# Performance work log

Measured on AMD Instinct MI355X. Metric: run time of the kernel, lower is better.

Reference implementation:

```python
import math
import jax, jax.numpy as jnp
import numpy as np

D_MODEL = 1024
D_CTX = 1024
NUM_HEADS = 16
ATTN_DIM = 1024
HEAD_DIM = ATTN_DIM // NUM_HEADS  # 64
ROPE_GAMMA = 10.0
ROTARY_BASE = 10000.0
ATTN_SCALE = math.sqrt(ATTN_DIM)  # note: module scales by sqrt(attn_dim), not sqrt(head_dim)


def _apply_rope(x, cos, sin):
    # x: [H,B,T,D]; cos/sin: [1,B,T,D//2]
    half = x.shape[-1] // 2
    x1, x2 = x[..., :half], x[..., half:]
    return jnp.concatenate([x1 * cos - x2 * sin, x1 * sin + x2 * cos], axis=-1)


def setup_inputs() -> dict:
    key = jax.random.key(0)
    ks = jax.random.split(key, 12)
    B, T, L = 4, 1024, 1024
    x = jax.random.normal(ks[0], (B, D_MODEL, T), jnp.float32)
    context = jax.random.normal(ks[1], (B, L, D_CTX), jnp.float32)
    # prefix (padding) masks with per-example valid lengths, as in real padded batches
    lens_q = jnp.array([1024, 896, 768, 640])
    lens_k = jnp.array([1024, 960, 832, 704])
    x_mask = (jnp.arange(T)[None, :] < lens_q[:, None]).astype(jnp.int32)[:, None, :]  # [B,1,T]
    context_mask = (jnp.arange(L)[None, :] < lens_k[:, None]).astype(jnp.int32)[:, None, :]  # [B,1,L]
    s = 0.02
    Wq = jax.random.normal(ks[2], (D_MODEL, ATTN_DIM), jnp.float32) * s
    bq = jax.random.normal(ks[3], (ATTN_DIM,), jnp.float32) * s
    Wk = jax.random.normal(ks[4], (D_CTX, ATTN_DIM), jnp.float32) * s
    bk = jax.random.normal(ks[5], (ATTN_DIM,), jnp.float32) * s
    Wv = jax.random.normal(ks[6], (D_CTX, ATTN_DIM), jnp.float32) * s
    bv = jax.random.normal(ks[7], (ATTN_DIM,), jnp.float32) * s
    Wo = jax.random.normal(ks[8], (ATTN_DIM, D_MODEL), jnp.float32) * s
    bo = jax.random.normal(ks[9], (D_MODEL,), jnp.float32) * s
    return {"x": x, "context": context, "x_mask": x_mask, "context_mask": context_mask,
            "Wq": Wq, "bq": bq, "Wk": Wk, "bk": bk, "Wv": Wv, "bv": bv, "Wo": Wo, "bo": bo}


def reference(x, context, x_mask, context_mask, Wq, bq, Wk, bk, Wv, bv, Wo, bo):
    B, _, T = x.shape
    L = context.shape[1]
    H, D = NUM_HEADS, HEAD_DIM
    xm = x_mask.astype(jnp.float32)          # [B,1,T]
    cmf = context_mask.astype(jnp.float32)   # [B,1,L]

    q = jnp.swapaxes(x, 1, 2) @ Wq + bq      # [B,T,attn_dim]
    k = context @ Wk + bk                    # [B,L,attn_dim]
    v = context @ Wv + bv                    # [B,L,attn_dim]

    q = q.reshape(B, T, H, D).transpose(2, 0, 1, 3)  # [H,B,T,D]
    k = k.reshape(B, L, H, D).transpose(2, 0, 1, 3)  # [H,B,L,D]
    v = v.reshape(B, L, H, D).transpose(2, 0, 1, 3)  # [H,B,L,D]

    # length-normalized RoPE (LARoPE)
    len_q = xm.sum(axis=(-2, -1)).reshape(-1, 1, 1)   # [B,1,1]
    len_k = cmf.sum(axis=(-2, -1)).reshape(-1, 1, 1)  # [B,1,1]
    pos_q = jnp.arange(T, dtype=jnp.float32).reshape(1, -1, 1)
    pos_k = jnp.arange(L, dtype=jnp.float32).reshape(1, -1, 1)
    inv_freq = 1.0 / (ROTARY_BASE ** (jnp.arange(0, D, 2, dtype=jnp.float32) / D))
    theta = (inv_freq * ROPE_GAMMA).reshape(1, 1, -1)  # [1,1,D//2]
    freqs_q = (pos_q / len_q) * theta  # [B,T,D//2]
    freqs_k = (pos_k / len_k) * theta  # [B,L,D//2]
    q = _apply_rope(q, jnp.cos(freqs_q)[None], jnp.sin(freqs_q)[None])
    k = _apply_rope(k, jnp.cos(freqs_k)[None], jnp.sin(freqs_k)[None])

    logits = jnp.einsum('hbtd,hbld->hbtl', q, k) / ATTN_SCALE  # [H,B,T,L]
    key_pad = (context_mask == 0)[None]  # [1,B,1,L]
    logits = jnp.where(key_pad, -jnp.inf, logits)
    attn = jax.nn.softmax(logits, axis=-1)
    query_pad = (x_mask == 0).transpose(1, 0, 2)[..., None]  # [1,B,T,1]
    attn = jnp.where(query_pad, 0.0, attn)

    out = jnp.einsum('hbtl,hbld->hbtd', attn, v)          # [H,B,T,D]
    out = out.transpose(1, 2, 0, 3).reshape(B, T, ATTN_DIM)
    out = out @ Wo + bo                                   # [B,T,d_model]
    out = out * jnp.swapaxes(xm, 1, 2)                    # [B,T,1] broadcast
    return jnp.swapaxes(out, 1, 2)                        # [B,d_model,T]
```

## Files before the change

### kernel.cpp

```cpp
#include <hip/hip_runtime.h>
#include <hip/hip_bf16.h>

typedef __attribute__((ext_vector_type(8))) short s8v;
typedef __attribute__((ext_vector_type(4))) float f4v;
typedef __attribute__((ext_vector_type(4))) unsigned short u4v;
typedef __attribute__((ext_vector_type(2))) unsigned int u2v;

#define NH 16

__device__ __forceinline__ unsigned short f2bf(float f) {
  union { float f; unsigned int u; } v; v.f = f;
  unsigned int r = (v.u + 0x7fffu + ((v.u >> 16) & 1u)) >> 16;
  return (unsigned short)r;
}
__device__ __forceinline__ void gll16(const void* g, void* l) {
  __builtin_amdgcn_global_load_lds((const __attribute__((address_space(1))) void*)g,
                                   (__attribute__((address_space(3))) void*)l, 16, 0, 0);
}
__device__ __forceinline__ unsigned int cvtpk(float lo, float hi) {
  unsigned int r;
  asm volatile("v_cvt_pk_bf16_f32 %0, %1, %2" : "=v"(r) : "v"(lo), "v"(hi));
  return r;
}

__global__ __launch_bounds__(256) void prep_kernel(
    const float* __restrict__ x, const float* __restrict__ ctx,
    const float* __restrict__ Wq, const float* __restrict__ Wk,
    const float* __restrict__ Wv, const float* __restrict__ Wo,
    const int* __restrict__ xm, const int* __restrict__ cm,
    unsigned short* __restrict__ xT, unsigned short* __restrict__ ctxb,
    unsigned short* __restrict__ WqT, unsigned short* __restrict__ WkT,
    unsigned short* __restrict__ WvT, unsigned short* __restrict__ WoT,
    float* __restrict__ lens, float2* __restrict__ rope) {
  const int z = blockIdx.z;
  const int tid = threadIdx.x;
  if (z == 12) {
    if (blockIdx.x | blockIdx.y) return;
    const int w = tid >> 6, lane = tid & 63;
    const int g = w * 2 + (lane >> 5);
    const int l32 = lane & 31;
    const int* m = (g < 4) ? (xm + g * 1024) : (cm + (g - 4) * 1024);
    int s = 0;
    for (int i = l32; i < 1024; i += 32) s += m[i];
    for (int o = 16; o; o >>= 1) s += __shfl_xor(s, o);
    if (l32 == 0) lens[g] = (float)s;
    return;
  }
  if (z == 13) {
    const int idx = blockIdx.y * 32 + blockIdx.x;
    if (idx >= 256) return;
    const int which = idx >> 7;
    const int b = (idx >> 5) & 3;
    const int t0 = (idx & 31) * 32;
    const int* m = (which ? cm : xm) + b * 1024;
    const int lane = tid & 63;
    int s = 0;
    for (int i = lane; i < 1024; i += 64) s += m[i];
    for (int o = 32; o; o >>= 1) s += __shfl_xor(s, o);
    const float len = (float)s;
    const int j = tid & 31;
    const float theta = 10.0f * __expf((float)j * -0.28782313662425572f);
    float2* rt = rope + ((size_t)(which * 4 + b) << 15);
    for (int it = 0; it < 4; ++it) {
      const int t = t0 + (tid >> 5) + it * 8;
      const float fr = (float)t / len * theta;
      float sn, cs;
      __sincosf(fr, &sn, &cs);
      rt[t * 32 + j] = make_float2(cs, sn);
    }
    return;
  }
  if (z >= 8) {
    const float* in = ctx + ((size_t)(z - 8) << 20);
    unsigned short* out = ctxb + ((size_t)(z - 8) << 20);
    const int i = (blockIdx.y * 32 + blockIdx.x) * 1024 + tid * 4;
    const f4v v = *(const f4v*)&in[i];
    u4v o;
#pragma unroll
    for (int j = 0; j < 4; ++j) o[j] = f2bf(v[j]);
    *(u4v*)&out[i] = o;
    return;
  }
  __shared__ unsigned short tile[32][33];
  const float* in;
  unsigned short* out;
  if (z < 4)      { in = x + ((size_t)z << 20); out = xT + ((size_t)z << 20); }
  else if (z == 4){ in = Wq; out = WqT; }
  else if (z == 5){ in = Wk; out = WkT; }
  else if (z == 6){ in = Wv; out = WvT; }
  else            { in = Wo; out = WoT; }
  const int r0 = blockIdx.y * 32, c0 = blockIdx.x * 32;
  const int tx = tid & 31, ty = tid >> 5;
  for (int i = ty; i < 32; i += 8) tile[i][tx] = f2bf(in[(size_t)(r0 + i) * 1024 + c0 + tx]);
  __syncthreads();
  for (int i = ty; i < 32; i += 8) out[(size_t)(c0 + i) * 1024 + r0 + tx] = tile[tx][i];
}

__global__ __launch_bounds__(256) void gemm_qkv_kernel(
    const unsigned short* __restrict__ xT, const unsigned short* __restrict__ ctxb,
    const unsigned short* __restrict__ WqT, const unsigned short* __restrict__ WkT,
    const unsigned short* __restrict__ WvT,
    const float* __restrict__ bq, const float* __restrict__ bk, const float* __restrict__ bv,
    unsigned short* __restrict__ Qb, unsigned short* __restrict__ Kb,
    unsigned short* __restrict__ Vtb, const float2* __restrict__ rope) {
  __shared__ __attribute__((aligned(16))) unsigned short As[8192];
  __shared__ __attribute__((aligned(16))) unsigned short Bs[8192];
  const int id = blockIdx.x + (blockIdx.y << 3) + (blockIdx.z << 8);
  const int rest = id >> 3;
  const int my = (id & 7) + ((rest & 3) << 3);
  const int nx = (rest >> 2) & 7;
  const int mode = rest >> 5;
  const unsigned short* A  = (mode == 0) ? xT : ctxb;
  const unsigned short* Bt = (mode == 0) ? WqT : (mode == 1) ? WkT : WvT;
  const float* bias        = (mode == 0) ? bq : (mode == 1) ? bk : bv;
  const int tid = threadIdx.x;
  const int lane = tid & 63, w = tid >> 6;
  const int lq = lane & 15, lg = lane >> 4;
  const int m0 = my * 128, n0 = nx * 128;
  const int wm = (w & 1) * 64, wn = (w >> 1) * 64;
  const int cswz = (lq & 7) << 3;
  f4v acc[4][4] = {};

  for (int kt = 0; kt < 16; ++kt) {
    const int k0 = kt * 64;
#pragma unroll
    for (int i = 0; i < 4; ++i) {
      const int ci = i * 256 + tid;
      const int row = ci >> 3;
      const int col = ((ci & 7) * 8) ^ ((row & 7) << 3);
      gll16(&A[(size_t)(m0 + row) * 1024 + k0 + col], &As[ci * 8]);
      gll16(&Bt[(size_t)(n0 + row) * 1024 + k0 + col], &Bs[ci * 8]);
    }
    __syncthreads();
#pragma unroll
    for (int kc = 0; kc < 2; ++kc) {
      s8v af[4], bfr[4];
#pragma unroll
      for (int i = 0; i < 4; ++i)
        af[i] = *(const s8v*)&As[(wm + i * 16 + lq) * 64 + ((kc * 32 + lg * 8) ^ cswz)];
#pragma unroll
      for (int i = 0; i < 4; ++i)
        bfr[i] = *(const s8v*)&Bs[(wn + i * 16 + lq) * 64 + ((kc * 32 + lg * 8) ^ cswz)];
#pragma unroll
      for (int mi = 0; mi < 4; ++mi)
#pragma unroll
        for (int ni = 0; ni < 4; ++ni)
          acc[mi][ni] = __builtin_amdgcn_mfma_f32_16x16x32_bf16(af[mi], bfr[ni], acc[mi][ni], 0, 0, 0);
    }
    __syncthreads();
  }

  float bv4[4];
#pragma unroll
  for (int ni = 0; ni < 4; ++ni) bv4[ni] = bias[n0 + wn + ni * 16 + lq];
  const int b = m0 >> 10;

  if (mode <= 1) {
    unsigned short* O = mode ? Kb : Qb;
    const float2* rt = rope + ((size_t)(mode * 4 + b) << 15);
    const int h = (n0 + wn) >> 6;
#pragma unroll
    for (int mi = 0; mi < 4; ++mi) {
#pragma unroll
      for (int rr = 0; rr < 4; ++rr) {
        const int m = m0 + wm + mi * 16 + lg * 4 + rr;
        const int t = m & 1023;
#pragma unroll
        for (int ni = 0; ni < 2; ++ni) {
          const int jj = ni * 16 + lq;
          const float2 cs2 = rt[t * 32 + jj];
          const float x1 = acc[mi][ni][rr] + bv4[ni];
          const float x2 = acc[mi][ni + 2][rr] + bv4[ni + 2];
          unsigned short* bp = &O[((size_t)((b * NH + h) * 1024 + t)) * 64 + jj];
          bp[0] = f2bf(x1 * cs2.x - x2 * cs2.y);
          bp[32] = f2bf(x1 * cs2.y + x2 * cs2.x);
        }
      }
    }
  } else {
#pragma unroll
    for (int mi = 0; mi < 4; ++mi) {
      const int mbase = m0 + wm + mi * 16 + lg * 4;
      const int l0 = mbase & 1023;
#pragma unroll
      for (int ni = 0; ni < 4; ++ni) {
        const int n = n0 + wn + ni * 16 + lq;
        const int hh = n >> 6, d = n & 63;
        u4v pk;
#pragma unroll
        for (int rr = 0; rr < 4; ++rr) pk[rr] = f2bf(acc[mi][ni][rr] + bv4[ni]);
        *(u4v*)&Vtb[((size_t)((b * NH + hh) * 64 + d)) * 1024 + l0] = pk;
      }
    }
  }
}

__global__ __launch_bounds__(256) void gemm_o_kernel(
    const unsigned short* __restrict__ A, const unsigned short* __restrict__ Bt,
    const float* __restrict__ bias, float* __restrict__ Cout,
    const int* __restrict__ xmask) {
  __shared__ __attribute__((aligned(16))) unsigned short As[8192];
  __shared__ __attribute__((aligned(16))) unsigned short Bs[8192];
  const int id = blockIdx.x + (blockIdx.y << 3);
  const int rest = id >> 3;
  const int my = (id & 7) + ((rest & 3) << 3);
  const int nx = rest >> 2;
  const int tid = threadIdx.x;
  const int lane = tid & 63, w = tid >> 6;
  const int lq = lane & 15, lg = lane >> 4;
  const int m0 = my * 128, n0 = nx * 128;
  const int wm = (w & 1) * 64, wn = (w >> 1) * 64;
  const int cswz = (lq & 7) << 3;
  f4v acc[4][4] = {};

  for (int kt = 0; kt < 16; ++kt) {
    const int k0 = kt * 64;
#pragma unroll
    for (int i = 0; i < 4; ++i) {
      const int ci = i * 256 + tid;
      const int row = ci >> 3;
      const int col = ((ci & 7) * 8) ^ ((row & 7) << 3);
      gll16(&A[(size_t)(m0 + row) * 1024 + k0 + col], &As[ci * 8]);
      gll16(&Bt[(size_t)(n0 + row) * 1024 + k0 + col], &Bs[ci * 8]);
    }
    __syncthreads();
#pragma unroll
    for (int kc = 0; kc < 2; ++kc) {
      s8v af[4], bfr[4];
#pragma unroll
      for (int i = 0; i < 4; ++i)
        af[i] = *(const s8v*)&As[(wm + i * 16 + lq) * 64 + ((kc * 32 + lg * 8) ^ cswz)];
#pragma unroll
      for (int i = 0; i < 4; ++i)
        bfr[i] = *(const s8v*)&Bs[(wn + i * 16 + lq) * 64 + ((kc * 32 + lg * 8) ^ cswz)];
#pragma unroll
      for (int mi = 0; mi < 4; ++mi)
#pragma unroll
        for (int ni = 0; ni < 4; ++ni)
          acc[mi][ni] = __builtin_amdgcn_mfma_f32_16x16x32_bf16(af[mi], bfr[ni], acc[mi][ni], 0, 0, 0);
    }
    __syncthreads();
  }

  float bv4[4];
#pragma unroll
  for (int ni = 0; ni < 4; ++ni) bv4[ni] = bias[n0 + wn + ni * 16 + lq];
  const int b = m0 >> 10;
#pragma unroll
  for (int mi = 0; mi < 4; ++mi) {
    const int mbase = m0 + wm + mi * 16 + lg * 4;
    const int t0 = mbase & 1023;
#pragma unroll
    for (int ni = 0; ni < 4; ++ni) {
      const int n = n0 + wn + ni * 16 + lq;
      f4v pk;
#pragma unroll
      for (int rr = 0; rr < 4; ++rr) {
        float v = acc[mi][ni][rr] + bv4[ni];
        v *= (float)xmask[b * 1024 + t0 + rr];
        pk[rr] = v;
      }
      *(f4v*)&Cout[(size_t)b * 1024 * 1024 + (size_t)n * 1024 + t0] = pk;
    }
  }
}

__global__ __launch_bounds__(512) void attn_kernel(
    const unsigned short* __restrict__ Q, const unsigned short* __restrict__ K,
    const unsigned short* __restrict__ Vt, const float* __restrict__ lens,
    unsigned short* __restrict__ Aout) {
  __shared__ __attribute__((aligned(16))) unsigned short Ks[2][4096];
  __shared__ __attribute__((aligned(16))) unsigned short Vs[2][4096];
  __shared__ __attribute__((aligned(16))) unsigned short Plds[8][16][72];
  const int tid = threadIdx.x;
  const int lane = tid & 63, w = tid >> 6;
  const int lq = lane & 15, lg = lane >> 4;
  const int id = blockIdx.x + (blockIdx.y << 3);
  const int bh = (id & 7) + (((id >> 3) & 7) << 3);
  const int qblk = id >> 6;
  const int b = bh >> 4, h = bh & 15;
  const int lenq = (int)lens[b];
  if (qblk * 128 >= lenq) return;
  const int lenk = (int)lens[4 + b];
  const int nkt = (lenk + 63) >> 6;
  const int qrow = qblk * 128 + w * 16;
  const unsigned short* Qp = Q + ((size_t)bh * 1024 + qrow) * 64;
  const unsigned short* Kp = K + (size_t)bh * 65536;
  const unsigned short* Vp = Vt + (size_t)bh * 65536;
  const s8v qf0 = *(const s8v*)&Qp[lq * 64 + lg * 8];
  const s8v qf1 = *(const s8v*)&Qp[lq * 64 + 32 + lg * 8];
  const int r0 = tid >> 3;
  const int c0x = ((tid & 7) * 8) ^ ((r0 & 7) << 3);
  const int cswz = (lq & 7) << 3;

  gll16(&Kp[(size_t)r0 * 64 + c0x], &Ks[0][tid * 8]);
  gll16(&Vp[(size_t)r0 * 1024 + c0x], &Vs[0][tid * 8]);
  __syncthreads();

  const float SC2 = 0.0450842200277f;
  float m_run = -1e30f, s_run = 0.0f;
  f4v ot[4] = {};
  for (int kt = 0; kt < nkt; ++kt) {
    const int p = kt & 1;
    if (kt + 1 < nkt) {
      const int kn = (kt + 1) * 64;
      gll16(&Kp[(size_t)(kn + r0) * 64 + c0x], &Ks[p ^ 1][tid * 8]);
      gll16(&Vp[(size_t)r0 * 1024 + kn + c0x], &Vs[p ^ 1][tid * 8]);
    }
    const int k0 = kt * 64;
    const bool full = (k0 + 64 <= lenk);
    float pvv[16];
    float tmax = -1e30f;
    __builtin_amdgcn_s_setprio(1);
#pragma unroll
    for (int kk = 0; kk < 4; ++kk) {
      const int krow = kk * 16 + lq;
      const s8v a0 = *(const s8v*)&Ks[p][krow * 64 + ((lg * 8) ^ cswz)];
      const s8v a1 = *(const s8v*)&Ks[p][krow * 64 + ((32 + lg * 8) ^ cswz)];
      f4v s = {};
      s = __builtin_amdgcn_mfma_f32_16x16x32_bf16(a0, qf0, s, 0, 0, 0);
      s = __builtin_amdgcn_mfma_f32_16x16x32_bf16(a1, qf1, s, 0, 0, 0);
#pragma unroll
      for (int rr = 0; rr < 4; ++rr) {
        float v = s[rr] * SC2;
        if (!full) {
          const int key = k0 + kk * 16 + lg * 4 + rr;
          if (key >= lenk) v = -1e30f;
        }
        pvv[kk * 4 + rr] = v;
        tmax = fmaxf(tmax, v);
      }
    }
    __builtin_amdgcn_s_setprio(0);
    tmax = fmaxf(tmax, __shfl_xor(tmax, 16));
    tmax = fmaxf(tmax, __shfl_xor(tmax, 32));
    if (__any(tmax > m_run + 8.0f)) {
      const float m_new = fmaxf(m_run, tmax);
      const float alpha = exp2f(m_run - m_new);
#pragma unroll
      for (int d = 0; d < 4; ++d)
#pragma unroll
        for (int j = 0; j < 4; ++j) ot[d][j] *= alpha;
      s_run *= alpha;
      m_run = m_new;
    }
    float psum = 0.0f;
#pragma unroll
    for (int kk = 0; kk < 4; ++kk) {
      const float e0 = exp2f(pvv[kk * 4 + 0] - m_run);
      const float e1 = exp2f(pvv[kk * 4 + 1] - m_run);
      const float e2 = exp2f(pvv[kk * 4 + 2] - m_run);
      const float e3 = exp2f(pvv[kk * 4 + 3] - m_run);
      psum += (e0 + e1) + (e2 + e3);
      u2v pw;
      pw[0] = cvtpk(e0, e1);
      pw[1] = cvtpk(e2, e3);
      *(u2v*)&Plds[w][lq][kk * 16 + lg * 4] = pw;
    }
    psum += __shfl_xor(psum, 16);
    psum += __shfl_xor(psum, 32);
    s_run += psum;
    const s8v pb0 = *(const s8v*)&Plds[w][lq][lg * 8];
    const s8v pb1 = *(const s8v*)&Plds[w][lq][32 + lg * 8];
    __builtin_amdgcn_s_setprio(1);
#pragma unroll
    for (int d = 0; d < 4; ++d) {
      const int vrow = d * 16 + lq;
      const s8v av0 = *(const s8v*)&Vs[p][vrow * 64 + ((lg * 8) ^ cswz)];
      const s8v av1 = *(const s8v*)&Vs[p][vrow * 64 + ((32 + lg * 8) ^ cswz)];
      ot[d] = __builtin_amdgcn_mfma_f32_16x16x32_bf16(av0, pb0, ot[d], 0, 0, 0);
      ot[d] = __builtin_amdgcn_mfma_f32_16x16x32_bf16(av1, pb1, ot[d], 0, 0, 0);
    }
    __builtin_amdgcn_s_setprio(0);
    if (kt + 1 < nkt) __syncthreads();
  }
  const float inv = 1.0f / s_run;
  const int t = qrow + lq;
  unsigned short* op = Aout + ((size_t)(b * 1024 + t)) * 1024 + h * 64;
#pragma unroll
  for (int d = 0; d < 4; ++d) {
    u4v oo;
#pragma unroll
    for (int rr = 0; rr < 4; ++rr) oo[rr] = f2bf(ot[d][rr] * inv);
    *(u4v*)&op[d * 16 + lg * 4] = oo;
  }
}

extern "C" void kernel_launch(void* const* d_in, const int* in_sizes, int n_in,
                              void* d_out, int out_size, void* d_ws, size_t ws_size,
                              hipStream_t stream) {
  const float* x   = (const float*)d_in[0];
  const float* ctx = (const float*)d_in[1];
  const int* xm = (const int*)d_in[2];
  const int* cm = (const int*)d_in[3];
  const float* Wq = (const float*)d_in[4];
  const float* bq = (const float*)d_in[5];
  const float* Wk = (const float*)d_in[6];
  const float* bk = (const float*)d_in[7];
  const float* Wv = (const float*)d_in[8];
  const float* bv = (const float*)d_in[9];
  const float* Wo = (const float*)d_in[10];
  const float* bo = (const float*)d_in[11];

  char* ws = (char*)d_ws;
  const size_t MB = 1024 * 1024;
  unsigned short* xT   = (unsigned short*)(ws);
  unsigned short* AOb  = (unsigned short*)(ws);
  unsigned short* ctxb = (unsigned short*)(ws + 8 * MB);
  unsigned short* WqT  = (unsigned short*)(ws + 16 * MB);
  unsigned short* WkT  = (unsigned short*)(ws + 18 * MB);
  unsigned short* WvT  = (unsigned short*)(ws + 20 * MB);
  unsigned short* WoT  = (unsigned short*)(ws + 22 * MB);
  unsigned short* Qb   = (unsigned short*)(ws + 24 * MB);
  unsigned short* Kb   = (unsigned short*)(ws + 32 * MB);
  unsigned short* Vtb  = (unsigned short*)(ws + 40 * MB);
  float* lens          = (float*)(ws + 48 * MB);
  float2* rope         = (float2*)(ws + 49 * MB);

  prep_kernel<<<dim3(32, 32, 14), 256, 0, stream>>>(x, ctx, Wq, Wk, Wv, Wo, xm, cm,
                                                    xT, ctxb, WqT, WkT, WvT, WoT, lens, rope);
  gemm_qkv_kernel<<<dim3(8, 32, 3), 256, 0, stream>>>(xT, ctxb, WqT, WkT, WvT,
                                                      bq, bk, bv, Qb, Kb, Vtb, rope);
  attn_kernel<<<dim3(8, 64), 512, 0, stream>>>(Qb, Kb, Vtb, lens, AOb);
  gemm_o_kernel<<<dim3(8, 32), 256, 0, stream>>>(AOb, WoT, bo, (float*)d_out, xm);
}
```

Before: 123.9 us.

## Double-buffer LDS tiles in QKV and output projection GEMMs

Both projection GEMM kernels now use two LDS buffers. The next K-tile's global-to-LDS loads are issued before the MFMA work on the current tile, so load latency can overlap with compute and one barrier per iteration is removed. LDS use per block doubles to 64KB, which may lower occupancy. Correctness relies on the remaining end-of-loop barrier and on the compiler waiting for the async loads before that barrier.

```diff
diff --git a/kernel.cpp b/kernel.cpp
--- a/kernel.cpp
+++ b/kernel.cpp
@@ -103,8 +103,8 @@
     const float* __restrict__ bq, const float* __restrict__ bk, const float* __restrict__ bv,
     unsigned short* __restrict__ Qb, unsigned short* __restrict__ Kb,
     unsigned short* __restrict__ Vtb, const float2* __restrict__ rope) {
-  __shared__ __attribute__((aligned(16))) unsigned short As[8192];
-  __shared__ __attribute__((aligned(16))) unsigned short Bs[8192];
+  __shared__ __attribute__((aligned(16))) unsigned short As[2][8192];
+  __shared__ __attribute__((aligned(16))) unsigned short Bs[2][8192];
   const int id = blockIdx.x + (blockIdx.y << 3) + (blockIdx.z << 8);
   const int rest = id >> 3;
   const int my = (id & 7) + ((rest & 3) << 3);
@@ -119,28 +119,38 @@
   const int m0 = my * 128, n0 = nx * 128;
   const int wm = (w & 1) * 64, wn = (w >> 1) * 64;
   const int cswz = (lq & 7) << 3;
+  const int srow = tid >> 3;
+  const int scol = ((tid & 7) * 8) ^ ((srow & 7) << 3);
+  const unsigned short* Ap = A + (size_t)(m0 + srow) * 1024 + scol;
+  const unsigned short* Bp = Bt + (size_t)(n0 + srow) * 1024 + scol;
   f4v acc[4][4] = {};
 
+#pragma unroll
+  for (int i = 0; i < 4; ++i) {
+    gll16(Ap + i * 32 * 1024, &As[0][(i * 256 + tid) * 8]);
+    gll16(Bp + i * 32 * 1024, &Bs[0][(i * 256 + tid) * 8]);
+  }
+  __syncthreads();
+
   for (int kt = 0; kt < 16; ++kt) {
-    const int k0 = kt * 64;
-#pragma unroll
-    for (int i = 0; i < 4; ++i) {
-      const int ci = i * 256 + tid;
-      const int row = ci >> 3;
-      const int col = ((ci & 7) * 8) ^ ((row & 7) << 3);
-      gll16(&A[(size_t)(m0 + row) * 1024 + k0 + col], &As[ci * 8]);
-      gll16(&Bt[(size_t)(n0 + row) * 1024 + k0 + col], &Bs[ci * 8]);
-    }
-    __syncthreads();
+    const int cur = kt & 1;
+    if (kt + 1 < 16) {
+      const int kn = (kt + 1) * 64;
+#pragma unroll
+      for (int i = 0; i < 4; ++i) {
+        gll16(Ap + i * 32 * 1024 + kn, &As[cur ^ 1][(i * 256 + tid) * 8]);
+        gll16(Bp + i * 32 * 1024 + kn, &Bs[cur ^ 1][(i * 256 + tid) * 8]);
+      }
+    }
 #pragma unroll
     for (int kc = 0; kc < 2; ++kc) {
       s8v af[4], bfr[4];
 #pragma unroll
       for (int i = 0; i < 4; ++i)
-        af[i] = *(const s8v*)&As[(wm + i * 16 + lq) * 64 + ((kc * 32 + lg * 8) ^ cswz)];
+        af[i] = *(const s8v*)&As[cur][(wm + i * 16 + lq) * 64 + ((kc * 32 + lg * 8) ^ cswz)];
 #pragma unroll
       for (int i = 0; i < 4; ++i)
-        bfr[i] = *(const s8v*)&Bs[(wn + i * 16 + lq) * 64 + ((kc * 32 + lg * 8) ^ cswz)];
+        bfr[i] = *(const s8v*)&Bs[cur][(wn + i * 16 + lq) * 64 + ((kc * 32 + lg * 8) ^ cswz)];
 #pragma unroll
       for (int mi = 0; mi < 4; ++mi)
 #pragma unroll
@@ -199,8 +209,8 @@
     const unsigned short* __restrict__ A, const unsigned short* __restrict__ Bt,
     const float* __restrict__ bias, float* __restrict__ Cout,
     const int* __restrict__ xmask) {
-  __shared__ __attribute__((aligned(16))) unsigned short As[8192];
-  __shared__ __attribute__((aligned(16))) unsigned short Bs[8192];
+  __shared__ __attribute__((aligned(16))) unsigned short As[2][8192];
+  __shared__ __attribute__((aligned(16))) unsigned short Bs[2][8192];
   const int id = blockIdx.x + (blockIdx.y << 3);
   const int rest = id >> 3;
   const int my = (id & 7) + ((rest & 3) << 3);
@@ -211,28 +221,38 @@
   const int m0 = my * 128, n0 = nx * 128;
   const int wm = (w & 1) * 64, wn = (w >> 1) * 64;
   const int cswz = (lq & 7) << 3;
+  const int srow = tid >> 3;
+  const int scol = ((tid & 7) * 8) ^ ((srow & 7) << 3);
+  const unsigned short* Ap = A + (size_t)(m0 + srow) * 1024 + scol;
+  const unsigned short* Bp = Bt + (size_t)(n0 + srow) * 1024 + scol;
   f4v acc[4][4] = {};
 
+#pragma unroll
+  for (int i = 0; i < 4; ++i) {
+    gll16(Ap + i * 32 * 1024, &As[0][(i * 256 + tid) * 8]);
+    gll16(Bp + i * 32 * 1024, &Bs[0][(i * 256 + tid) * 8]);
+  }
+  __syncthreads();
+
   for (int kt = 0; kt < 16; ++kt) {
-    const int k0 = kt * 64;
-#pragma unroll
-    for (int i = 0; i < 4; ++i) {
-      const int ci = i * 256 + tid;
-      const int row = ci >> 3;
-      const int col = ((ci & 7) * 8) ^ ((row & 7) << 3);
-      gll16(&A[(size_t)(m0 + row) * 1024 + k0 + col], &As[ci * 8]);
-      gll16(&Bt[(size_t)(n0 + row) * 1024 + k0 + col], &Bs[ci * 8]);
-    }
-    __syncthreads();
+    const int cur = kt & 1;
+    if (kt + 1 < 16) {
+      const int kn = (kt + 1) * 64;
+#pragma unroll
+      for (int i = 0; i < 4; ++i) {
+        gll16(Ap + i * 32 * 1024 + kn, &As[cur ^ 1][(i * 256 + tid) * 8]);
+        gll16(Bp + i * 32 * 1024 + kn, &Bs[cur ^ 1][(i * 256 + tid) * 8]);
+      }
+    }
 #pragma unroll
     for (int kc = 0; kc < 2; ++kc) {
       s8v af[4], bfr[4];
 #pragma unroll
       for (int i = 0; i < 4; ++i)
-        af[i] = *(const s8v*)&As[(wm + i * 16 + lq) * 64 + ((kc * 32 + lg * 8) ^ cswz)];
+        af[i] = *(const s8v*)&As[cur][(wm + i * 16 + lq) * 64 + ((kc * 32 + lg * 8) ^ cswz)];
 #pragma unroll
       for (int i = 0; i < 4; ++i)
-        bfr[i] = *(const s8v*)&Bs[(wn + i * 16 + lq) * 64 + ((kc * 32 + lg * 8) ^ cswz)];
+        bfr[i] = *(const s8v*)&Bs[cur][(wn + i * 16 + lq) * 64 + ((kc * 32 + lg * 8) ^ cswz)];
 #pragma unroll
       for (int mi = 0; mi < 4; ++mi)
 #pragma unroll
```

After: 124.7 us. About the same (+0.6%).
